# Kernel tuning notes

Hardware: AMD Instinct MI355X
Metric: run time of the kernel (lower is better)

Reference implementation:

```python
import jax, jax.numpy as jnp
import numpy as np

V, C, T_BLK, H, L = 65, 512, 256, 8, 8
HS = C // H
EPS = 1e-5


def _ln(x, g, b):
    m = jnp.mean(x, axis=-1, keepdims=True)
    v = jnp.mean((x - m) ** 2, axis=-1, keepdims=True)
    return (x - m) * jax.lax.rsqrt(v + EPS) * g + b


def setup_inputs() -> dict:
    key = jax.random.key(0)
    ks = jax.random.split(key, 16)
    B, T = 64, 256
    idx = jax.random.randint(ks[0], (B, T), 0, V)
    targets = jax.random.randint(ks[1], (B, T), 0, V)
    n = lambda k, shape, s: (jax.random.normal(k, shape, dtype=jnp.float32) * s)
    return {
        "idx": idx,
        "targets": targets,
        "tok_emb": n(ks[2], (V, C), 0.02),
        "pos_emb": n(ks[3], (T_BLK, C), 0.02),
        "ln1_g": jnp.ones((L, C), jnp.float32),
        "ln1_b": jnp.zeros((L, C), jnp.float32),
        "wq": n(ks[4], (L, C, C), (2.0 / C) ** 0.5),
        "wk": n(ks[5], (L, C, C), (2.0 / C) ** 0.5),
        "wv": n(ks[6], (L, C, C), (2.0 / C) ** 0.5),
        "wo": n(ks[7], (L, C, C), (2.0 / C) ** 0.5),
        "bo": jnp.zeros((L, C), jnp.float32),
        "ln2_g": jnp.ones((L, C), jnp.float32),
        "ln2_b": jnp.zeros((L, C), jnp.float32),
        "w1": n(ks[8], (L, C, 4 * C), (2.0 / C) ** 0.5),
        "b1": jnp.zeros((L, 4 * C), jnp.float32),
        "w2": n(ks[9], (L, 4 * C, C), (2.0 / (4 * C)) ** 0.5),
        "b2": jnp.zeros((L, C), jnp.float32),
        "lnf_g": jnp.ones((C,), jnp.float32),
        "lnf_b": jnp.zeros((C,), jnp.float32),
        "lm_w": n(ks[10], (C, V), (2.0 / C) ** 0.5),
        "lm_b": jnp.zeros((V,), jnp.float32),
    }


def _gpt_forward(tok_emb, pos_emb, ln1_g, ln1_b, wq, wk, wv, wo, bo,
                 ln2_g, ln2_b, w1, b1, w2, b2, lnf_g, lnf_b, lm_w, lm_b,
                 idx, targets):
    B, T = idx.shape
    x = tok_emb[idx] + pos_emb[:T]  # [B,T,C]
    causal = jnp.tril(jnp.ones((T, T), bool))
    scale = float(C) ** -0.5  # NOTE: scaled by n_embd, not head_size (faithful)
    for l in range(L):
        h = _ln(x, ln1_g[l], ln1_b[l])
        q = (h @ wq[l]).reshape(B, T, H, HS)
        k = (h @ wk[l]).reshape(B, T, H, HS)
        v = (h @ wv[l]).reshape(B, T, H, HS)
        scores = jnp.einsum('bthd,bshd->bhts', q, k) * scale
        scores = jnp.where(causal, scores, -jnp.inf)
        w = jax.nn.softmax(scores, axis=-1)
        attn = jnp.einsum('bhts,bshd->bthd', w, v).reshape(B, T, C)
        x = x + attn @ wo[l] + bo[l]
        h2 = _ln(x, ln2_g[l], ln2_b[l])
        x = x + jax.nn.relu(h2 @ w1[l] + b1[l]) @ w2[l] + b2[l]
    x = _ln(x, lnf_g, lnf_b)
    logits = (x @ lm_w + lm_b).reshape(B * T, V)
    logp = jax.nn.log_softmax(logits, axis=-1)
    tgt = targets.reshape(B * T)
    loss = -jnp.mean(jnp.take_along_axis(logp, tgt[:, None], axis=-1))
    return logits, loss


def reference(idx, targets, tok_emb, pos_emb, ln1_g, ln1_b, wq, wk, wv, wo, bo,
              ln2_g, ln2_b, w1, b1, w2, b2, lnf_g, lnf_b, lm_w, lm_b):
    return _gpt_forward(tok_emb, pos_emb, ln1_g, ln1_b, wq, wk, wv, wo, bo,
                        ln2_g, ln2_b, w1, b1, w2, b2, lnf_g, lnf_b, lm_w, lm_b,
                        idx, targets)
```

## Files before the change

kernel.cpp:

```cpp
#include <hip/hip_runtime.h>
#include <math.h>

#define V_SZ   65
#define C_DIM  512
#define T_SEQ  256
#define H_N    8
#define HS_D   64
#define L_N    8
#define N_TOK  16384
#define LN_EPS 1e-5f
#define SM_SCALE 0.044194173824159216f

typedef unsigned short ushortT;
typedef __attribute__((ext_vector_type(8))) short    short8;
typedef __attribute__((ext_vector_type(8))) ushortT  ushort8;
typedef __attribute__((ext_vector_type(4))) float    f32x4;

typedef __attribute__((address_space(3))) unsigned int        lds_uint;
typedef const __attribute__((address_space(1))) unsigned int  glob_uint;

__device__ inline ushortT f2bf(float f) {
    unsigned int u = __float_as_uint(f);
    u = (u + 0x7fffu + ((u >> 16) & 1u)) >> 16;
    return (ushortT)u;
}
__device__ inline float bf2f(ushortT u) {
    return __uint_as_float(((unsigned int)u) << 16);
}

__global__ void embed_kernel(const int* __restrict__ idx,
                             const float* __restrict__ tok,
                             const float* __restrict__ pos,
                             float* __restrict__ x) {
    int i = blockIdx.x * blockDim.x + threadIdx.x;
    const int NF4 = N_TOK * C_DIM / 4;
    if (i >= NF4) return;
    int c4 = i % (C_DIM / 4);
    int n  = i / (C_DIM / 4);
    int t  = n % T_SEQ;
    int tk = idx[n];
    float4 a = ((const float4*)tok)[(size_t)tk * (C_DIM/4) + c4];
    float4 p = ((const float4*)pos)[(size_t)t  * (C_DIM/4) + c4];
    float4 r; r.x=a.x+p.x; r.y=a.y+p.y; r.z=a.z+p.z; r.w=a.w+p.w;
    ((float4*)x)[i] = r;
}

__global__ __launch_bounds__(256) void tcast_kernel(const float* __restrict__ src,
                                                    ushortT* __restrict__ dst,
                                                    int K, int N) {
    __shared__ float tile[32][33];
    size_t lo = (size_t)blockIdx.z * K * N;
    int n0 = blockIdx.x * 32, k0 = blockIdx.y * 32;
    int tx = threadIdx.x & 31, ty = threadIdx.x >> 5;
    #pragma unroll
    for (int s = 0; s < 4; s++) {
        int kk = ty + s * 8;
        tile[kk][tx] = src[lo + (size_t)(k0 + kk) * N + n0 + tx];
    }
    __syncthreads();
    #pragma unroll
    for (int s = 0; s < 4; s++) {
        int nn = ty + s * 8;
        dst[lo + (size_t)(n0 + nn) * K + k0 + tx] = f2bf(tile[tx][nn]);
    }
}

__global__ __launch_bounds__(256) void lmcast_kernel(const float* __restrict__ w,
                                                     ushortT* __restrict__ dst) {
    int n = blockIdx.x;
    for (int k = threadIdx.x; k < C_DIM; k += 256)
        dst[(size_t)n * C_DIM + k] = (n < V_SZ) ? f2bf(w[(size_t)k * V_SZ + n]) : (ushortT)0;
}

template<bool BF16OUT>
__global__ __launch_bounds__(256) void ln_kernel(const float* __restrict__ in,
                                                 const float* __restrict__ g,
                                                 const float* __restrict__ b,
                                                 void* __restrict__ outv) {
    int wave = threadIdx.x >> 6;
    int lane = threadIdx.x & 63;
    int row  = blockIdx.x * 4 + wave;
    const float4* r4 = (const float4*)(in + (size_t)row * C_DIM);
    float v[8];
    *(float4*)&v[0] = r4[lane * 2];
    *(float4*)&v[4] = r4[lane * 2 + 1];
    float s = 0.f;
    #pragma unroll
    for (int k = 0; k < 8; k++) s += v[k];
    #pragma unroll
    for (int m = 32; m >= 1; m >>= 1) s += __shfl_xor(s, m, 64);
    float mean = s * (1.0f / C_DIM);
    float vs = 0.f;
    #pragma unroll
    for (int k = 0; k < 8; k++) { float d = v[k] - mean; vs += d * d; }
    #pragma unroll
    for (int m = 32; m >= 1; m >>= 1) vs += __shfl_xor(vs, m, 64);
    float rstd = rsqrtf(vs * (1.0f / C_DIM) + LN_EPS);
    float gv[8], bv[8];
    *(float4*)&gv[0] = *(const float4*)&g[lane * 8];
    *(float4*)&gv[4] = *(const float4*)&g[lane * 8 + 4];
    *(float4*)&bv[0] = *(const float4*)&b[lane * 8];
    *(float4*)&bv[4] = *(const float4*)&b[lane * 8 + 4];
    if (BF16OUT) {
        ushort8 pack;
        #pragma unroll
        for (int k = 0; k < 8; k++) pack[k] = f2bf((v[k] - mean) * rstd * gv[k] + bv[k]);
        *(ushort8*)&((ushortT*)outv)[(size_t)row * C_DIM + lane * 8] = pack;
    } else {
        float o[8];
        #pragma unroll
        for (int k = 0; k < 8; k++) o[k] = (v[k] - mean) * rstd * gv[k] + bv[k];
        float4* o4 = (float4*)&((float*)outv)[(size_t)row * C_DIM + lane * 8];
        o4[0] = *(float4*)&o[0];
        o4[1] = *(float4*)&o[4];
    }
}

template<int EPI>
__device__ __forceinline__ void gemm_core(const ushortT* __restrict__ A,
                                          const ushortT* __restrict__ Bt,
                                          const float* __restrict__ bias,
                                          const float* __restrict__ res,
                                          void* __restrict__ outp,
                                          int N, int K,
                                          int mBase, int nBase) {
    __shared__ __align__(16) ushortT As[128 * 32];
    __shared__ __align__(16) ushortT Bs[128 * 32];
    const int tid = threadIdx.x;
    const int w = tid >> 6, lane = tid & 63;
    const int wr = w >> 1, wc = w & 1;
    const int l15 = lane & 15, lg = lane >> 4;

    const int srow = (lane >> 2);
    const int sslot = lane & 3;

    f32x4 acc[4][4];
    #pragma unroll
    for (int i = 0; i < 4; i++)
        #pragma unroll
        for (int j = 0; j < 4; j++)
            acc[i][j] = {0.f, 0.f, 0.f, 0.f};

    for (int k0 = 0; k0 < K; k0 += 32) {
        #pragma unroll
        for (int t = 0; t < 2; t++) {
            int r = w * 32 + t * 16 + srow;
            int ks = sslot ^ ((r >> 1) & 3);
            const ushortT* ga = &A[(size_t)(mBase + r) * K + k0 + ks * 8];
            __builtin_amdgcn_global_load_lds((glob_uint*)ga,
                (lds_uint*)&As[(w * 32 + t * 16) * 32], 16, 0, 0);
            const ushortT* gb = &Bt[(size_t)(nBase + r) * K + k0 + ks * 8];
            __builtin_amdgcn_global_load_lds((glob_uint*)gb,
                (lds_uint*)&Bs[(w * 32 + t * 16) * 32], 16, 0, 0);
        }
        __syncthreads();
        short8 af[4], bfr[4];
        #pragma unroll
        for (int i = 0; i < 4; i++) {
            int r = wr * 64 + i * 16 + l15;
            int cb = (lg * 16) ^ (((r >> 1) & 3) << 4);
            af[i] = *(const short8*)((const char*)As + r * 64 + cb);
        }
        #pragma unroll
        for (int j = 0; j < 4; j++) {
            int r = wc * 64 + j * 16 + l15;
            int cb = (lg * 16) ^ (((r >> 1) & 3) << 4);
            bfr[j] = *(const short8*)((const char*)Bs + r * 64 + cb);
        }
        #pragma unroll
        for (int i = 0; i < 4; i++)
            #pragma unroll
            for (int j = 0; j < 4; j++)
                acc[i][j] = __builtin_amdgcn_mfma_f32_16x16x32_bf16(af[i], bfr[j], acc[i][j], 0, 0, 0);
        __syncthreads();
    }

    int lr = lg * 4;
    #pragma unroll
    for (int i = 0; i < 4; i++) {
        #pragma unroll
        for (int j = 0; j < 4; j++) {
            int col = nBase + wc * 64 + j * 16 + l15;
            if (EPI == 4 && col >= V_SZ) continue;
            #pragma unroll
            for (int q = 0; q < 4; q++) {
                size_t row = (size_t)(mBase + wr * 64 + i * 16 + lr + q);
                float vv = acc[i][j][q];
                if (EPI >= 2) vv += bias[col];
                if (EPI == 2) vv = fmaxf(vv, 0.f);
                if (EPI == 3) vv += res[row * N + col];
                if (EPI == 1)      ((ushortT*)outp)[row * N + col] = f2bf(vv);
                else if (EPI == 2) ((ushortT*)outp)[row * N + col] = f2bf(vv);
                else if (EPI == 3) ((float*)outp)[row * N + col]   = vv;
                else               ((float*)outp)[row * V_SZ + col] = vv;
            }
        }
    }
}

template<int EPI>
__global__ __launch_bounds__(256, 2) void gemm_bf16(const ushortT* __restrict__ A,
                                                    const ushortT* __restrict__ Bt,
                                                    const float* __restrict__ bias,
                                                    const float* __restrict__ res,
                                                    void* __restrict__ outp,
                                                    int N, int K) {
    gemm_core<EPI>(A, Bt, bias, res, outp, N, K, blockIdx.x * 128, blockIdx.y * 128);
}

__global__ __launch_bounds__(256, 2) void gemm_qkv(const ushortT* __restrict__ A,
                                                   const ushortT* __restrict__ bq,
                                                   const ushortT* __restrict__ bk,
                                                   const ushortT* __restrict__ bv,
                                                   ushortT* __restrict__ oq,
                                                   ushortT* __restrict__ ok,
                                                   ushortT* __restrict__ ov,
                                                   int N, int K) {
    const ushortT* Bt = (blockIdx.z == 0) ? bq : (blockIdx.z == 1) ? bk : bv;
    ushortT*       o  = (blockIdx.z == 0) ? oq : (blockIdx.z == 1) ? ok : ov;
    gemm_core<1>(A, Bt, nullptr, nullptr, o, N, K, blockIdx.x * 128, blockIdx.y * 128);
}

__global__ __launch_bounds__(256) void attn_kernel(const ushortT* __restrict__ qp,
                                                   const ushortT* __restrict__ kp,
                                                   const ushortT* __restrict__ vp,
                                                   ushortT* __restrict__ att) {
    __shared__ ushortT K_lds[T_SEQ][72];
    __shared__ ushortT Vt_lds[HS_D][264];
    __shared__ ushortT P_lds[4][16][72];
    int bh = blockIdx.x;
    int b = bh >> 3, h = bh & 7;
    int tid = threadIdx.x;
    int w = tid >> 6, lane = tid & 63;
    const size_t rowbase = (size_t)b * T_SEQ * C_DIM + (size_t)h * HS_D;
    int l15 = lane & 15, lg = lane >> 4;

    #pragma unroll
    for (int it = 0; it < 8; it++) {
        int f = tid + it * 256;
        int r = f >> 3, c8 = f & 7;
        ushort8 kb = *(const ushort8*)&kp[rowbase + (size_t)r * C_DIM + c8 * 8];
        *(ushort8*)&K_lds[r][c8 * 8] = kb;
        ushort8 vb = *(const ushort8*)&vp[rowbase + (size_t)r * C_DIM + c8 * 8];
        #pragma unroll
        for (int e = 0; e < 8; e++) Vt_lds[c8 * 8 + e][r] = vb[e];
    }

    short8 qf[4][2];
    #pragma unroll
    for (int i = 0; i < 4; i++) {
        int grow = 16 * (4 * i + w) + l15;
        #pragma unroll
        for (int kk = 0; kk < 2; kk++)
            qf[i][kk] = *(const short8*)&qp[rowbase + (size_t)grow * C_DIM + kk * 32 + lg * 8];
    }
    __syncthreads();

    f32x4 acc_o[4][4];
    float mrun[4][4], lrun[4][4];
    #pragma unroll
    for (int i = 0; i < 4; i++) {
        #pragma unroll
        for (int j = 0; j < 4; j++) acc_o[i][j] = {0.f, 0.f, 0.f, 0.f};
        #pragma unroll
        for (int q = 0; q < 4; q++) { mrun[i][q] = -1e30f; lrun[i][q] = 0.f; }
    }

    #pragma unroll
    for (int jt = 0; jt < 4; jt++) {
        #pragma unroll
        for (int i = 0; i < 4; i++) {
            if (i < jt) continue;
            f32x4 acc_s[4];
            #pragma unroll
            for (int j_ = 0; j_ < 4; j_++) acc_s[j_] = {0.f, 0.f, 0.f, 0.f};
            #pragma unroll
            for (int j_ = 0; j_ < 4; j_++)
                #pragma unroll
                for (int kk = 0; kk < 2; kk++) {
                    short8 kf = *(const short8*)&K_lds[jt * 64 + j_ * 16 + l15][kk * 32 + lg * 8];
                    acc_s[j_] = __builtin_amdgcn_mfma_f32_16x16x32_bf16(qf[i][kk], kf, acc_s[j_], 0, 0, 0);
                }
            float sv[4][4];
            #pragma unroll
            for (int j_ = 0; j_ < 4; j_++) {
                int colg = jt * 64 + j_ * 16 + l15;
                #pragma unroll
                for (int q = 0; q < 4; q++) {
                    int rowg = 16 * (4 * i + w) + lg * 4 + q;
                    float s = acc_s[j_][q] * SM_SCALE;
                    sv[j_][q] = (i == jt && colg > rowg) ? -1e30f : s;
                }
            }
            #pragma unroll
            for (int q = 0; q < 4; q++) {
                float mx = fmaxf(fmaxf(sv[0][q], sv[1][q]), fmaxf(sv[2][q], sv[3][q]));
                #pragma unroll
                for (int msk = 1; msk <= 8; msk <<= 1) mx = fmaxf(mx, __shfl_xor(mx, msk, 64));
                float mold = mrun[i][q];
                float mnew = fmaxf(mold, mx);
                float corr = __expf(mold - mnew);
                mrun[i][q] = mnew;
                float ps = 0.f;
                #pragma unroll
                for (int j_ = 0; j_ < 4; j_++) {
                    float pe = __expf(sv[j_][q] - mnew);
                    ps += pe;
                    P_lds[w][lg * 4 + q][j_ * 16 + l15] = f2bf(pe);
                }
                lrun[i][q] = lrun[i][q] * corr + ps;
                #pragma unroll
                for (int dj = 0; dj < 4; dj++) acc_o[i][dj][q] *= corr;
            }
            short8 pa[2];
            #pragma unroll
            for (int kk = 0; kk < 2; kk++)
                pa[kk] = *(const short8*)&P_lds[w][l15][kk * 32 + lg * 8];
            #pragma unroll
            for (int dj = 0; dj < 4; dj++)
                #pragma unroll
                for (int kk = 0; kk < 2; kk++) {
                    short8 vf = *(const short8*)&Vt_lds[dj * 16 + l15][jt * 64 + kk * 32 + lg * 8];
                    acc_o[i][dj] = __builtin_amdgcn_mfma_f32_16x16x32_bf16(pa[kk], vf, acc_o[i][dj], 0, 0, 0);
                }
        }
    }

    #pragma unroll
    for (int i = 0; i < 4; i++) {
        float inv[4];
        #pragma unroll
        for (int q = 0; q < 4; q++) {
            float ls = lrun[i][q];
            #pragma unroll
            for (int msk = 1; msk <= 8; msk <<= 1) ls += __shfl_xor(ls, msk, 64);
            inv[q] = 1.0f / ls;
        }
        #pragma unroll
        for (int dj = 0; dj < 4; dj++) {
            int colg = dj * 16 + l15;
            #pragma unroll
            for (int q = 0; q < 4; q++) {
                int rowg = 16 * (4 * i + w) + lg * 4 + q;
                att[rowbase + (size_t)rowg * C_DIM + colg] = f2bf(acc_o[i][dj][q] * inv[q]);
            }
        }
    }
}

__global__ __launch_bounds__(256) void rowloss_kernel(const float* __restrict__ logits,
                                                      const int* __restrict__ tgt,
                                                      float* __restrict__ rl) {
    int wave = threadIdx.x >> 6, lane = threadIdx.x & 63;
    int n = blockIdx.x * 4 + wave;
    const float* l = logits + (size_t)n * V_SZ;
    float v0 = l[lane];
    float v1 = (lane == 0) ? l[64] : -1e30f;
    float m = fmaxf(v0, v1);
    #pragma unroll
    for (int s = 32; s >= 1; s >>= 1) m = fmaxf(m, __shfl_xor(m, s, 64));
    float e = __expf(v0 - m) + ((lane == 0) ? __expf(v1 - m) : 0.f);
    #pragma unroll
    for (int s = 32; s >= 1; s >>= 1) e += __shfl_xor(e, s, 64);
    if (lane == 0) {
        float lp = l[tgt[n]] - m - logf(e);
        rl[n] = -lp;
    }
}

__global__ __launch_bounds__(256) void reduce_loss_kernel(const float* __restrict__ rl,
                                                          float* __restrict__ out_loss) {
    __shared__ float sdata[256];
    float s = 0.f;
    for (int i = threadIdx.x; i < N_TOK; i += 256) s += rl[i];
    sdata[threadIdx.x] = s;
    __syncthreads();
    for (int st = 128; st > 0; st >>= 1) {
        if (threadIdx.x < st) sdata[threadIdx.x] += sdata[threadIdx.x + st];
        __syncthreads();
    }
    if (threadIdx.x == 0) out_loss[0] = sdata[0] * (1.0f / N_TOK);
}

extern "C" void kernel_launch(void* const* d_in, const int* in_sizes, int n_in,
                              void* d_out, int out_size, void* d_ws, size_t ws_size,
                              hipStream_t stream) {
    const int*   idx     = (const int*)d_in[0];
    const int*   targets = (const int*)d_in[1];
    const float* tok_emb = (const float*)d_in[2];
    const float* pos_emb = (const float*)d_in[3];
    const float* ln1_g   = (const float*)d_in[4];
    const float* ln1_b   = (const float*)d_in[5];
    const float* wq      = (const float*)d_in[6];
    const float* wk      = (const float*)d_in[7];
    const float* wv      = (const float*)d_in[8];
    const float* wo      = (const float*)d_in[9];
    const float* bo      = (const float*)d_in[10];
    const float* ln2_g   = (const float*)d_in[11];
    const float* ln2_b   = (const float*)d_in[12];
    const float* w1      = (const float*)d_in[13];
    const float* b1      = (const float*)d_in[14];
    const float* w2      = (const float*)d_in[15];
    const float* b2      = (const float*)d_in[16];
    const float* lnf_g   = (const float*)d_in[17];
    const float* lnf_b   = (const float*)d_in[18];
    const float* lm_w    = (const float*)d_in[19];
    const float* lm_b    = (const float*)d_in[20];

    float* out = (float*)d_out;
    char*  ws  = (char*)d_ws;
    const size_t MB = 1024ull * 1024ull;
    float*   x     = (float*)(ws);
    ushortT* h_bf  = (ushortT*)(ws + 32 * MB);
    ushortT* q_bf  = (ushortT*)(ws + 48 * MB);
    ushortT* k_bf  = (ushortT*)(ws + 64 * MB);
    ushortT* v_bf  = (ushortT*)(ws + 80 * MB);
    ushortT* att_bf= (ushortT*)(ws + 112 * MB);
    ushortT* ff1_bf= (ushortT*)(ws + 48 * MB);
    ushortT* wqT   = (ushortT*)(ws + 128 * MB);
    ushortT* wkT   = (ushortT*)(ws + 132 * MB);
    ushortT* wvT   = (ushortT*)(ws + 136 * MB);
    ushortT* woT   = (ushortT*)(ws + 140 * MB);
    ushortT* w1T   = (ushortT*)(ws + 144 * MB);
    ushortT* w2T   = (ushortT*)(ws + 160 * MB);
    float*   rl    = (float*)(ws + 176 * MB);
    ushortT* lmT   = (ushortT*)(ws + 177 * MB);

    {
        dim3 gCC(C_DIM / 32, C_DIM / 32, L_N);
        tcast_kernel<<<gCC, 256, 0, stream>>>(wq, wqT, C_DIM, C_DIM);
        tcast_kernel<<<gCC, 256, 0, stream>>>(wk, wkT, C_DIM, C_DIM);
        tcast_kernel<<<gCC, 256, 0, stream>>>(wv, wvT, C_DIM, C_DIM);
        tcast_kernel<<<gCC, 256, 0, stream>>>(wo, woT, C_DIM, C_DIM);
        dim3 g1(4 * C_DIM / 32, C_DIM / 32, L_N);
        tcast_kernel<<<g1, 256, 0, stream>>>(w1, w1T, C_DIM, 4 * C_DIM);
        dim3 g2(C_DIM / 32, 4 * C_DIM / 32, L_N);
        tcast_kernel<<<g2, 256, 0, stream>>>(w2, w2T, 4 * C_DIM, C_DIM);
        lmcast_kernel<<<128, 256, 0, stream>>>(lm_w, lmT);
    }

    embed_kernel<<<(N_TOK * C_DIM / 4 + 255) / 256, 256, 0, stream>>>(idx, tok_emb, pos_emb, x);

    dim3 gemmCC(N_TOK / 128, C_DIM / 128);
    dim3 gemmC4(N_TOK / 128, 4 * C_DIM / 128);
    dim3 gemmQKV(N_TOK / 128, C_DIM / 128, 3);

    for (int l = 0; l < L_N; l++) {
        const ushortT* wqT_l = wqT + (size_t)l * C_DIM * C_DIM;
        const ushortT* wkT_l = wkT + (size_t)l * C_DIM * C_DIM;
        const ushortT* wvT_l = wvT + (size_t)l * C_DIM * C_DIM;
        const ushortT* woT_l = woT + (size_t)l * C_DIM * C_DIM;
        const ushortT* w1T_l = w1T + (size_t)l * C_DIM * 4 * C_DIM;
        const ushortT* w2T_l = w2T + (size_t)l * C_DIM * 4 * C_DIM;

        ln_kernel<true><<<N_TOK / 4, 256, 0, stream>>>(x, ln1_g + l * C_DIM, ln1_b + l * C_DIM, h_bf);
        gemm_qkv<<<gemmQKV, 256, 0, stream>>>(h_bf, wqT_l, wkT_l, wvT_l, q_bf, k_bf, v_bf, C_DIM, C_DIM);
        attn_kernel<<<64 * H_N, 256, 0, stream>>>(q_bf, k_bf, v_bf, att_bf);
        gemm_bf16<3><<<gemmCC, 256, 0, stream>>>(att_bf, woT_l, bo + l * C_DIM, x, x, C_DIM, C_DIM);
        ln_kernel<true><<<N_TOK / 4, 256, 0, stream>>>(x, ln2_g + l * C_DIM, ln2_b + l * C_DIM, h_bf);
        gemm_bf16<2><<<gemmC4, 256, 0, stream>>>(h_bf, w1T_l, b1 + (size_t)l * 4 * C_DIM, nullptr, ff1_bf, 4 * C_DIM, C_DIM);
        gemm_bf16<3><<<gemmCC, 256, 0, stream>>>(ff1_bf, w2T_l, b2 + l * C_DIM, x, x, C_DIM, 4 * C_DIM);
    }

    ln_kernel<true><<<N_TOK / 4, 256, 0, stream>>>(x, lnf_g, lnf_b, h_bf);
    gemm_bf16<4><<<dim3(N_TOK / 128, 1), 256, 0, stream>>>(h_bf, lmT, lm_b, nullptr, out, V_SZ, C_DIM);

    rowloss_kernel<<<N_TOK / 4, 256, 0, stream>>>(out, targets, rl);
    reduce_loss_kernel<<<1, 256, 0, stream>>>(rl, out + (size_t)N_TOK * V_SZ);
}
```

Measured before the change: 1.728 ms.

## Replace 128x128 GEMMs with 256x256-tile 4-stage pipelined MFMA GEMM

Result: slower. 1.858 ms (+7.5%).

```diff
diff --git a/kernel.cpp b/kernel.cpp
--- a/kernel.cpp
+++ b/kernel.cpp
@@ -116,21 +116,264 @@
     }
 }
 
+__device__ __forceinline__ void stage_half(const ushortT* __restrict__ X,
+                                           ushortT* lds_slot,
+                                           int rBase, int K, int kt,
+                                           int w, int lane, int j) {
+    int r = w * 32 + j * 16 + (lane >> 2);
+    int g = (lane & 3) ^ ((r >> 1) & 3);
+    const ushortT* src = &X[(size_t)(rBase + r) * K + kt * 32 + g * 8];
+    __builtin_amdgcn_global_load_lds((glob_uint*)src,
+        (lds_uint*)&lds_slot[(w * 32 + j * 16) * 32], 16, 0, 0);
+}
+
 template<int EPI>
-__device__ __forceinline__ void gemm_core(const ushortT* __restrict__ A,
-                                          const ushortT* __restrict__ Bt,
-                                          const float* __restrict__ bias,
-                                          const float* __restrict__ res,
-                                          void* __restrict__ outp,
-                                          int N, int K,
-                                          int mBase, int nBase) {
+__global__ __launch_bounds__(512, 2) void gemm256(const ushortT* __restrict__ A,
+                                                  const ushortT* __restrict__ Bt,
+                                                  const float* __restrict__ bias,
+                                                  const float* __restrict__ res,
+                                                  void* __restrict__ outp,
+                                                  int N, int K) {
+    __shared__ __align__(16) ushortT As[4][256 * 32];
+    __shared__ __align__(16) ushortT Bs[4][256 * 32];
+    const int tid = threadIdx.x;
+    const int w = tid >> 6, lane = tid & 63;
+    const int wm = w >> 2, wn = w & 3;
+    const int l15 = lane & 15, lg = lane >> 4;
+    const int mBase = blockIdx.x * 256, nBase = blockIdx.y * 256;
+    const int NT = K >> 5;
+
+    f32x4 acc[8][4];
+    #pragma unroll
+    for (int i = 0; i < 8; i++)
+        #pragma unroll
+        for (int j = 0; j < 4; j++)
+            acc[i][j] = {0.f, 0.f, 0.f, 0.f};
+
+    #pragma unroll
+    for (int kt = 0; kt < 3; kt++) {
+        stage_half(A,  As[kt & 3], mBase, K, kt, w, lane, 0);
+        stage_half(A,  As[kt & 3], mBase, K, kt, w, lane, 1);
+        stage_half(Bt, Bs[kt & 3], nBase, K, kt, w, lane, 0);
+        stage_half(Bt, Bs[kt & 3], nBase, K, kt, w, lane, 1);
+    }
+
+    for (int kt = 0; kt < NT; kt++) {
+        if (kt + 3 <= NT)      asm volatile("s_waitcnt vmcnt(8)" ::: "memory");
+        else if (kt + 2 == NT) asm volatile("s_waitcnt vmcnt(4)" ::: "memory");
+        else                   asm volatile("s_waitcnt vmcnt(0)" ::: "memory");
+        __builtin_amdgcn_s_barrier();
+        __builtin_amdgcn_sched_barrier(0);
+
+        const ushortT* as = &As[kt & 3][0];
+        const ushortT* bs = &Bs[kt & 3][0];
+        const bool st = (kt + 3 < NT);
+
+        short8 bfrag[4], afrag[4];
+        #pragma unroll
+        for (int fc = 0; fc < 4; fc++) {
+            int r = wn * 64 + fc * 16 + l15;
+            int g = lg ^ ((r >> 1) & 3);
+            bfrag[fc] = *(const short8*)&bs[r * 32 + g * 8];
+        }
+        #pragma unroll
+        for (int fr = 0; fr < 4; fr++) {
+            int r = wm * 128 + fr * 16 + l15;
+            int g = lg ^ ((r >> 1) & 3);
+            afrag[fr] = *(const short8*)&as[r * 32 + g * 8];
+        }
+        if (st) {
+            stage_half(A, As[(kt + 3) & 3], mBase, K, kt + 3, w, lane, 0);
+            stage_half(A, As[(kt + 3) & 3], mBase, K, kt + 3, w, lane, 1);
+        }
+        asm volatile("s_waitcnt lgkmcnt(0)" ::: "memory");
+        __builtin_amdgcn_sched_barrier(0);
+        __builtin_amdgcn_s_setprio(1);
+        #pragma unroll
+        for (int fr = 0; fr < 4; fr++)
+            #pragma unroll
+            for (int fc = 0; fc < 4; fc++)
+                acc[fr][fc] = __builtin_amdgcn_mfma_f32_16x16x32_bf16(afrag[fr], bfrag[fc], acc[fr][fc], 0, 0, 0);
+        __builtin_amdgcn_s_setprio(0);
+
+        short8 afrag2[4];
+        #pragma unroll
+        for (int fr = 0; fr < 4; fr++) {
+            int r = wm * 128 + (fr + 4) * 16 + l15;
+            int g = lg ^ ((r >> 1) & 3);
+            afrag2[fr] = *(const short8*)&as[r * 32 + g * 8];
+        }
+        if (st) {
+            stage_half(Bt, Bs[(kt + 3) & 3], nBase, K, kt + 3, w, lane, 0);
+            stage_half(Bt, Bs[(kt + 3) & 3], nBase, K, kt + 3, w, lane, 1);
+        }
+        asm volatile("s_waitcnt lgkmcnt(0)" ::: "memory");
+        __builtin_amdgcn_sched_barrier(0);
+        __builtin_amdgcn_s_setprio(1);
+        #pragma unroll
+        for (int fr = 0; fr < 4; fr++)
+            #pragma unroll
+            for (int fc = 0; fc < 4; fc++)
+                acc[fr + 4][fc] = __builtin_amdgcn_mfma_f32_16x16x32_bf16(afrag2[fr], bfrag[fc], acc[fr + 4][fc], 0, 0, 0);
+        __builtin_amdgcn_s_setprio(0);
+    }
+
+    int lr = lg * 4;
+    #pragma unroll
+    for (int fr = 0; fr < 8; fr++) {
+        #pragma unroll
+        for (int fc = 0; fc < 4; fc++) {
+            int col = nBase + wn * 64 + fc * 16 + l15;
+            #pragma unroll
+            for (int q = 0; q < 4; q++) {
+                size_t row = (size_t)(mBase + wm * 128 + fr * 16 + lr + q);
+                float vv = acc[fr][fc][q];
+                if (EPI >= 2) vv += bias[col];
+                if (EPI == 2) vv = fmaxf(vv, 0.f);
+                if (EPI == 3) vv += res[row * N + col];
+                if (EPI == 1)      ((ushortT*)outp)[row * N + col] = f2bf(vv);
+                else if (EPI == 2) ((ushortT*)outp)[row * N + col] = f2bf(vv);
+                else               ((float*)outp)[row * N + col]   = vv;
+            }
+        }
+    }
+}
+
+__global__ __launch_bounds__(512, 2) void gemm256_qkv(const ushortT* __restrict__ A,
+                                                      const ushortT* __restrict__ bq,
+                                                      const ushortT* __restrict__ bk,
+                                                      const ushortT* __restrict__ bv,
+                                                      ushortT* __restrict__ oq,
+                                                      ushortT* __restrict__ ok,
+                                                      ushortT* __restrict__ ov,
+                                                      int N, int K);
+
+template<int EPI>
+__device__ __forceinline__ void gemm256_body(const ushortT* A, const ushortT* Bt,
+                                             const float* bias, const float* res,
+                                             void* outp, int N, int K);
+
+__global__ __launch_bounds__(512, 2) void gemm256_sel(const ushortT* __restrict__ A,
+                                                      const ushortT* __restrict__ b0,
+                                                      const ushortT* __restrict__ b1,
+                                                      const ushortT* __restrict__ b2,
+                                                      ushortT* __restrict__ o0,
+                                                      ushortT* __restrict__ o1,
+                                                      ushortT* __restrict__ o2,
+                                                      int N, int K) {
+    __shared__ __align__(16) ushortT As[4][256 * 32];
+    __shared__ __align__(16) ushortT Bs[4][256 * 32];
+    const ushortT* Bt = (blockIdx.z == 0) ? b0 : (blockIdx.z == 1) ? b1 : b2;
+    ushortT*       op = (blockIdx.z == 0) ? o0 : (blockIdx.z == 1) ? o1 : o2;
+    const int tid = threadIdx.x;
+    const int w = tid >> 6, lane = tid & 63;
+    const int wm = w >> 2, wn = w & 3;
+    const int l15 = lane & 15, lg = lane >> 4;
+    const int mBase = blockIdx.x * 256, nBase = blockIdx.y * 256;
+    const int NT = K >> 5;
+
+    f32x4 acc[8][4];
+    #pragma unroll
+    for (int i = 0; i < 8; i++)
+        #pragma unroll
+        for (int j = 0; j < 4; j++)
+            acc[i][j] = {0.f, 0.f, 0.f, 0.f};
+
+    #pragma unroll
+    for (int kt = 0; kt < 3; kt++) {
+        stage_half(A,  As[kt & 3], mBase, K, kt, w, lane, 0);
+        stage_half(A,  As[kt & 3], mBase, K, kt, w, lane, 1);
+        stage_half(Bt, Bs[kt & 3], nBase, K, kt, w, lane, 0);
+        stage_half(Bt, Bs[kt & 3], nBase, K, kt, w, lane, 1);
+    }
+
+    for (int kt = 0; kt < NT; kt++) {
+        if (kt + 3 <= NT)      asm volatile("s_waitcnt vmcnt(8)" ::: "memory");
+        else if (kt + 2 == NT) asm volatile("s_waitcnt vmcnt(4)" ::: "memory");
+        else                   asm volatile("s_waitcnt vmcnt(0)" ::: "memory");
+        __builtin_amdgcn_s_barrier();
+        __builtin_amdgcn_sched_barrier(0);
+
+        const ushortT* as = &As[kt & 3][0];
+        const ushortT* bs = &Bs[kt & 3][0];
+        const bool st = (kt + 3 < NT);
+
+        short8 bfrag[4], afrag[4];
+        #pragma unroll
+        for (int fc = 0; fc < 4; fc++) {
+            int r = wn * 64 + fc * 16 + l15;
+            int g = lg ^ ((r >> 1) & 3);
+            bfrag[fc] = *(const short8*)&bs[r * 32 + g * 8];
+        }
+        #pragma unroll
+        for (int fr = 0; fr < 4; fr++) {
+            int r = wm * 128 + fr * 16 + l15;
+            int g = lg ^ ((r >> 1) & 3);
+            afrag[fr] = *(const short8*)&as[r * 32 + g * 8];
+        }
+        if (st) {
+            stage_half(A, As[(kt + 3) & 3], mBase, K, kt + 3, w, lane, 0);
+            stage_half(A, As[(kt + 3) & 3], mBase, K, kt + 3, w, lane, 1);
+        }
+        asm volatile("s_waitcnt lgkmcnt(0)" ::: "memory");
+        __builtin_amdgcn_sched_barrier(0);
+        __builtin_amdgcn_s_setprio(1);
+        #pragma unroll
+        for (int fr = 0; fr < 4; fr++)
+            #pragma unroll
+            for (int fc = 0; fc < 4; fc++)
+                acc[fr][fc] = __builtin_amdgcn_mfma_f32_16x16x32_bf16(afrag[fr], bfrag[fc], acc[fr][fc], 0, 0, 0);
+        __builtin_amdgcn_s_setprio(0);
+
+        short8 afrag2[4];
+        #pragma unroll
+        for (int fr = 0; fr < 4; fr++) {
+            int r = wm * 128 + (fr + 4) * 16 + l15;
+            int g = lg ^ ((r >> 1) & 3);
+            afrag2[fr] = *(const short8*)&as[r * 32 + g * 8];
+        }
+        if (st) {
+            stage_half(Bt, Bs[(kt + 3) & 3], nBase, K, kt + 3, w, lane, 0);
+            stage_half(Bt, Bs[(kt + 3) & 3], nBase, K, kt + 3, w, lane, 1);
+        }
+        asm volatile("s_waitcnt lgkmcnt(0)" ::: "memory");
+        __builtin_amdgcn_sched_barrier(0);
+        __builtin_amdgcn_s_setprio(1);
+        #pragma unroll
+        for (int fr = 0; fr < 4; fr++)
+            #pragma unroll
+            for (int fc = 0; fc < 4; fc++)
+                acc[fr + 4][fc] = __builtin_amdgcn_mfma_f32_16x16x32_bf16(afrag2[fr], bfrag[fc], acc[fr + 4][fc], 0, 0, 0);
+        __builtin_amdgcn_s_setprio(0);
+    }
+
+    int lr = lg * 4;
+    #pragma unroll
+    for (int fr = 0; fr < 8; fr++) {
+        #pragma unroll
+        for (int fc = 0; fc < 4; fc++) {
+            int col = nBase + wn * 64 + fc * 16 + l15;
+            #pragma unroll
+            for (int q = 0; q < 4; q++) {
+                size_t row = (size_t)(mBase + wm * 128 + fr * 16 + lr + q);
+                op[row * N + col] = f2bf(acc[fr][fc][q]);
+            }
+        }
+    }
+}
+
+__global__ __launch_bounds__(256, 2) void gemm_lm(const ushortT* __restrict__ A,
+                                                  const ushortT* __restrict__ Bt,
+                                                  const float* __restrict__ bias,
+                                                  float* __restrict__ outp,
+                                                  int K) {
     __shared__ __align__(16) ushortT As[128 * 32];
     __shared__ __align__(16) ushortT Bs[128 * 32];
     const int tid = threadIdx.x;
     const int w = tid >> 6, lane = tid & 63;
     const int wr = w >> 1, wc = w & 1;
     const int l15 = lane & 15, lg = lane >> 4;
-
+    const int mBase = blockIdx.x * 128, nBase = 0;
     const int srow = (lane >> 2);
     const int sslot = lane & 3;
 
@@ -181,44 +424,14 @@
         #pragma unroll
         for (int j = 0; j < 4; j++) {
             int col = nBase + wc * 64 + j * 16 + l15;
-            if (EPI == 4 && col >= V_SZ) continue;
+            if (col >= V_SZ) continue;
             #pragma unroll
             for (int q = 0; q < 4; q++) {
                 size_t row = (size_t)(mBase + wr * 64 + i * 16 + lr + q);
-                float vv = acc[i][j][q];
-                if (EPI >= 2) vv += bias[col];
-                if (EPI == 2) vv = fmaxf(vv, 0.f);
-                if (EPI == 3) vv += res[row * N + col];
-                if (EPI == 1)      ((ushortT*)outp)[row * N + col] = f2bf(vv);
-                else if (EPI == 2) ((ushortT*)outp)[row * N + col] = f2bf(vv);
-                else if (EPI == 3) ((float*)outp)[row * N + col]   = vv;
-                else               ((float*)outp)[row * V_SZ + col] = vv;
+                outp[row * V_SZ + col] = acc[i][j][q] + bias[col];
             }
         }
     }
-}
-
-template<int EPI>
-__global__ __launch_bounds__(256, 2) void gemm_bf16(const ushortT* __restrict__ A,
-                                                    const ushortT* __restrict__ Bt,
-                                                    const float* __restrict__ bias,
-                                                    const float* __restrict__ res,
-                                                    void* __restrict__ outp,
-                                                    int N, int K) {
-    gemm_core<EPI>(A, Bt, bias, res, outp, N, K, blockIdx.x * 128, blockIdx.y * 128);
-}
-
-__global__ __launch_bounds__(256, 2) void gemm_qkv(const ushortT* __restrict__ A,
-                                                   const ushortT* __restrict__ bq,
-                                                   const ushortT* __restrict__ bk,
-                                                   const ushortT* __restrict__ bv,
-                                                   ushortT* __restrict__ oq,
-                                                   ushortT* __restrict__ ok,
-                                                   ushortT* __restrict__ ov,
-                                                   int N, int K) {
-    const ushortT* Bt = (blockIdx.z == 0) ? bq : (blockIdx.z == 1) ? bk : bv;
-    ushortT*       o  = (blockIdx.z == 0) ? oq : (blockIdx.z == 1) ? ok : ov;
-    gemm_core<1>(A, Bt, nullptr, nullptr, o, N, K, blockIdx.x * 128, blockIdx.y * 128);
 }
 
 __global__ __launch_bounds__(256) void attn_kernel(const ushortT* __restrict__ qp,
@@ -441,9 +654,9 @@
 
     embed_kernel<<<(N_TOK * C_DIM / 4 + 255) / 256, 256, 0, stream>>>(idx, tok_emb, pos_emb, x);
 
-    dim3 gemmCC(N_TOK / 128, C_DIM / 128);
-    dim3 gemmC4(N_TOK / 128, 4 * C_DIM / 128);
-    dim3 gemmQKV(N_TOK / 128, C_DIM / 128, 3);
+    dim3 g256CC(N_TOK / 256, C_DIM / 256);
+    dim3 g256C4(N_TOK / 256, 4 * C_DIM / 256);
+    dim3 g256QKV(N_TOK / 256, C_DIM / 256, 3);
 
     for (int l = 0; l < L_N; l++) {
         const ushortT* wqT_l = wqT + (size_t)l * C_DIM * C_DIM;
@@ -454,16 +667,16 @@
         const ushortT* w2T_l = w2T + (size_t)l * C_DIM * 4 * C_DIM;
 
         ln_kernel<true><<<N_TOK / 4, 256, 0, stream>>>(x, ln1_g + l * C_DIM, ln1_b + l * C_DIM, h_bf);
-        gemm_qkv<<<gemmQKV, 256, 0, stream>>>(h_bf, wqT_l, wkT_l, wvT_l, q_bf, k_bf, v_bf, C_DIM, C_DIM);
+        gemm256_sel<<<g256QKV, 512, 0, stream>>>(h_bf, wqT_l, wkT_l, wvT_l, q_bf, k_bf, v_bf, C_DIM, C_DIM);
         attn_kernel<<<64 * H_N, 256, 0, stream>>>(q_bf, k_bf, v_bf, att_bf);
-        gemm_bf16<3><<<gemmCC, 256, 0, stream>>>(att_bf, woT_l, bo + l * C_DIM, x, x, C_DIM, C_DIM);
+        gemm256<3><<<g256CC, 512, 0, stream>>>(att_bf, woT_l, bo + l * C_DIM, x, x, C_DIM, C_DIM);
         ln_kernel<true><<<N_TOK / 4, 256, 0, stream>>>(x, ln2_g + l * C_DIM, ln2_b + l * C_DIM, h_bf);
-        gemm_bf16<2><<<gemmC4, 256, 0, stream>>>(h_bf, w1T_l, b1 + (size_t)l * 4 * C_DIM, nullptr, ff1_bf, 4 * C_DIM, C_DIM);
-        gemm_bf16<3><<<gemmCC, 256, 0, stream>>>(ff1_bf, w2T_l, b2 + l * C_DIM, x, x, C_DIM, 4 * C_DIM);
+        gemm256<2><<<g256C4, 512, 0, stream>>>(h_bf, w1T_l, b1 + (size_t)l * 4 * C_DIM, nullptr, ff1_bf, 4 * C_DIM, C_DIM);
+        gemm256<3><<<g256CC, 512, 0, stream>>>(ff1_bf, w2T_l, b2 + l * C_DIM, x, x, C_DIM, 4 * C_DIM);
     }
 
     ln_kernel<true><<<N_TOK / 4, 256, 0, stream>>>(x, lnf_g, lnf_b, h_bf);
-    gemm_bf16<4><<<dim3(N_TOK / 128, 1), 256, 0, stream>>>(h_bf, lmT, lm_b, nullptr, out, V_SZ, C_DIM);
+    gemm_lm<<<N_TOK / 128, 256, 0, stream>>>(h_bf, lmT, lm_b, out, C_DIM);
 
     rowloss_kernel<<<N_TOK / 4, 256, 0, stream>>>(out, targets, rl);
     reduce_loss_kernel<<<1, 256, 0, stream>>>(rl, out + (size_t)N_TOK * V_SZ);
```

## Double-buffer GEMM LDS tiles to overlap global loads with MFMA

Applied to the files above, without the earlier changes.

Measured after the change: 1.751 ms. About the same (+1.4%).

```diff
diff --git a/kernel.cpp b/kernel.cpp
--- a/kernel.cpp
+++ b/kernel.cpp
@@ -124,14 +124,13 @@
                                           void* __restrict__ outp,
                                           int N, int K,
                                           int mBase, int nBase) {
-    __shared__ __align__(16) ushortT As[128 * 32];
-    __shared__ __align__(16) ushortT Bs[128 * 32];
+    __shared__ __align__(16) ushortT As[2][128 * 32];
+    __shared__ __align__(16) ushortT Bs[2][128 * 32];
     const int tid = threadIdx.x;
     const int w = tid >> 6, lane = tid & 63;
     const int wr = w >> 1, wc = w & 1;
     const int l15 = lane & 15, lg = lane >> 4;
-
-    const int srow = (lane >> 2);
+    const int srow = lane >> 2;
     const int sslot = lane & 3;
 
     f32x4 acc[4][4];
@@ -141,38 +140,53 @@
         for (int j = 0; j < 4; j++)
             acc[i][j] = {0.f, 0.f, 0.f, 0.f};
 
-    for (int k0 = 0; k0 < K; k0 += 32) {
+    auto stage = [&](int buf, int k0) {
         #pragma unroll
         for (int t = 0; t < 2; t++) {
             int r = w * 32 + t * 16 + srow;
             int ks = sslot ^ ((r >> 1) & 3);
             const ushortT* ga = &A[(size_t)(mBase + r) * K + k0 + ks * 8];
             __builtin_amdgcn_global_load_lds((glob_uint*)ga,
-                (lds_uint*)&As[(w * 32 + t * 16) * 32], 16, 0, 0);
+                (lds_uint*)&As[buf][(w * 32 + t * 16) * 32], 16, 0, 0);
             const ushortT* gb = &Bt[(size_t)(nBase + r) * K + k0 + ks * 8];
             __builtin_amdgcn_global_load_lds((glob_uint*)gb,
-                (lds_uint*)&Bs[(w * 32 + t * 16) * 32], 16, 0, 0);
-        }
-        __syncthreads();
+                (lds_uint*)&Bs[buf][(w * 32 + t * 16) * 32], 16, 0, 0);
+        }
+    };
+
+    stage(0, 0);
+    asm volatile("s_waitcnt vmcnt(0)" ::: "memory");
+    __builtin_amdgcn_s_barrier();
+
+    int cur = 0;
+    for (int k0 = 0; k0 < K; k0 += 32) {
+        if (k0 + 32 < K) stage(cur ^ 1, k0 + 32);
+
         short8 af[4], bfr[4];
         #pragma unroll
         for (int i = 0; i < 4; i++) {
             int r = wr * 64 + i * 16 + l15;
             int cb = (lg * 16) ^ (((r >> 1) & 3) << 4);
-            af[i] = *(const short8*)((const char*)As + r * 64 + cb);
+            af[i] = *(const short8*)((const char*)&As[cur][0] + r * 64 + cb);
         }
         #pragma unroll
         for (int j = 0; j < 4; j++) {
             int r = wc * 64 + j * 16 + l15;
             int cb = (lg * 16) ^ (((r >> 1) & 3) << 4);
-            bfr[j] = *(const short8*)((const char*)Bs + r * 64 + cb);
-        }
+            bfr[j] = *(const short8*)((const char*)&Bs[cur][0] + r * 64 + cb);
+        }
+        asm volatile("s_waitcnt lgkmcnt(0)" ::: "memory");
+        __builtin_amdgcn_sched_barrier(0);
+        __builtin_amdgcn_s_setprio(1);
         #pragma unroll
         for (int i = 0; i < 4; i++)
             #pragma unroll
             for (int j = 0; j < 4; j++)
                 acc[i][j] = __builtin_amdgcn_mfma_f32_16x16x32_bf16(af[i], bfr[j], acc[i][j], 0, 0, 0);
-        __syncthreads();
+        __builtin_amdgcn_s_setprio(0);
+        asm volatile("s_waitcnt vmcnt(0)" ::: "memory");
+        __builtin_amdgcn_s_barrier();
+        cur ^= 1;
     }
 
     int lr = lg * 4;
```

## Triple-buffer GEMM LDS tiles with async prefetch two stages ahead

Applied to the files above, without the earlier changes.

Result: slower. 1.787 ms (+3.5%).

```diff
diff --git a/kernel.cpp b/kernel.cpp
--- a/kernel.cpp
+++ b/kernel.cpp
@@ -124,15 +124,15 @@
                                           void* __restrict__ outp,
                                           int N, int K,
                                           int mBase, int nBase) {
-    __shared__ __align__(16) ushortT As[128 * 32];
-    __shared__ __align__(16) ushortT Bs[128 * 32];
+    __shared__ __align__(16) ushortT As[3][128 * 32];
+    __shared__ __align__(16) ushortT Bs[3][128 * 32];
     const int tid = threadIdx.x;
     const int w = tid >> 6, lane = tid & 63;
     const int wr = w >> 1, wc = w & 1;
     const int l15 = lane & 15, lg = lane >> 4;
-
-    const int srow = (lane >> 2);
+    const int srow = lane >> 2;
     const int sslot = lane & 3;
+    const int NT = K >> 5;
 
     f32x4 acc[4][4];
     #pragma unroll
@@ -141,38 +141,51 @@
         for (int j = 0; j < 4; j++)
             acc[i][j] = {0.f, 0.f, 0.f, 0.f};
 
-    for (int k0 = 0; k0 < K; k0 += 32) {
+    auto stage = [&](int slot, int k0) {
         #pragma unroll
         for (int t = 0; t < 2; t++) {
             int r = w * 32 + t * 16 + srow;
             int ks = sslot ^ ((r >> 1) & 3);
             const ushortT* ga = &A[(size_t)(mBase + r) * K + k0 + ks * 8];
             __builtin_amdgcn_global_load_lds((glob_uint*)ga,
-                (lds_uint*)&As[(w * 32 + t * 16) * 32], 16, 0, 0);
+                (lds_uint*)&As[slot][(w * 32 + t * 16) * 32], 16, 0, 0);
             const ushortT* gb = &Bt[(size_t)(nBase + r) * K + k0 + ks * 8];
             __builtin_amdgcn_global_load_lds((glob_uint*)gb,
-                (lds_uint*)&Bs[(w * 32 + t * 16) * 32], 16, 0, 0);
-        }
-        __syncthreads();
+                (lds_uint*)&Bs[slot][(w * 32 + t * 16) * 32], 16, 0, 0);
+        }
+    };
+
+    stage(0, 0);
+    stage(1, 32);
+
+    for (int t = 0; t < NT; t++) {
+        if (t + 1 < NT) asm volatile("s_waitcnt vmcnt(4)" ::: "memory");
+        else            asm volatile("s_waitcnt vmcnt(0)" ::: "memory");
+        asm volatile("s_barrier" ::: "memory");
+        if (t + 2 < NT) stage((t + 2) % 3, (t + 2) * 32);
+
+        const char* as = (const char*)&As[t % 3][0];
+        const char* bs = (const char*)&Bs[t % 3][0];
         short8 af[4], bfr[4];
         #pragma unroll
         for (int i = 0; i < 4; i++) {
             int r = wr * 64 + i * 16 + l15;
             int cb = (lg * 16) ^ (((r >> 1) & 3) << 4);
-            af[i] = *(const short8*)((const char*)As + r * 64 + cb);
+            af[i] = *(const short8*)(as + r * 64 + cb);
         }
         #pragma unroll
         for (int j = 0; j < 4; j++) {
             int r = wc * 64 + j * 16 + l15;
             int cb = (lg * 16) ^ (((r >> 1) & 3) << 4);
-            bfr[j] = *(const short8*)((const char*)Bs + r * 64 + cb);
-        }
+            bfr[j] = *(const short8*)(bs + r * 64 + cb);
+        }
+        __builtin_amdgcn_s_setprio(1);
         #pragma unroll
         for (int i = 0; i < 4; i++)
             #pragma unroll
             for (int j = 0; j < 4; j++)
                 acc[i][j] = __builtin_amdgcn_mfma_f32_16x16x32_bf16(af[i], bfr[j], acc[i][j], 0, 0, 0);
-        __syncthreads();
+        __builtin_amdgcn_s_setprio(0);
     }
 
     int lr = lg * 4;
@@ -199,7 +212,7 @@
 }
 
 template<int EPI>
-__global__ __launch_bounds__(256, 2) void gemm_bf16(const ushortT* __restrict__ A,
+__global__ __launch_bounds__(256, 3) void gemm_bf16(const ushortT* __restrict__ A,
                                                     const ushortT* __restrict__ Bt,
                                                     const float* __restrict__ bias,
                                                     const float* __restrict__ res,
@@ -208,7 +221,7 @@
     gemm_core<EPI>(A, Bt, bias, res, outp, N, K, blockIdx.x * 128, blockIdx.y * 128);
 }
 
-__global__ __launch_bounds__(256, 2) void gemm_qkv(const ushortT* __restrict__ A,
+__global__ __launch_bounds__(256, 3) void gemm_qkv(const ushortT* __restrict__ A,
                                                    const ushortT* __restrict__ bq,
                                                    const ushortT* __restrict__ bk,
                                                    const ushortT* __restrict__ bv,
```
